# Performance work log

Hardware: AMD Instinct MI355X
Metric: run time of the kernel (lower is better)

The kernel has to match this reference:

```python
import jax, jax.numpy as jnp
import numpy as np

NQ = 6          # num_qubits
BS = 3          # basis_size (Pauli x,y,z)
HID = 32        # LSTM hidden size
SNAPS = 16      # max_num_snapshots
BATCH = 1024
DIM = 2 ** NQ   # 64


def _pauli():
    sx = np.array([[0., 1.], [1., 0.]], dtype=np.complex64)
    sy = np.array([[0., -1j], [1j, 0.]], dtype=np.complex64)
    sz = np.array([[1., 0.], [0., -1.]], dtype=np.complex64)
    return np.stack([sx, sy, sz], axis=0)


def setup_inputs():
    key = jax.random.key(0)
    ks = jax.random.split(key, 12)
    snapshot = jax.random.uniform(ks[0], (BATCH, NQ), jnp.float32, -1.0, 1.0)
    basis_comp_vector = jax.nn.softmax(
        jax.random.normal(ks[1], (BATCH, NQ, BS), jnp.float32), axis=-1)
    # valid density matrices: rho = A A^dag / tr
    ar = jax.random.normal(ks[2], (BATCH, DIM, DIM), jnp.float32)
    ai = jax.random.normal(ks[3], (BATCH, DIM, DIM), jnp.float32)
    A = ar + 1j * ai
    rho_c = jnp.einsum('bij,bkj->bik', A, jnp.conj(A))
    tr = jnp.trace(rho_c, axis1=1, axis2=2)[:, None, None]
    rho_c = rho_c / tr
    rho = jnp.stack([jnp.real(rho_c), jnp.imag(rho_c)], axis=1).astype(jnp.float32)
    h0 = jax.random.normal(ks[4], (BATCH, HID), jnp.float32)
    c0 = jax.random.normal(ks[5], (BATCH, HID), jnp.float32)
    in_dim = NQ + NQ * BS
    W_ih = jax.random.normal(ks[6], (4 * HID, in_dim), jnp.float32) * 0.1
    W_hh = jax.random.normal(ks[7], (4 * HID, HID), jnp.float32) * 0.1
    b_ih = jax.random.normal(ks[8], (4 * HID,), jnp.float32) * 0.05
    b_hh = jax.random.normal(ks[9], (4 * HID,), jnp.float32) * 0.05
    Wp = jax.random.normal(ks[10], (NQ, HID, BS), jnp.float32) * 0.1
    bp = jax.random.normal(ks[11], (NQ, BS), jnp.float32) * 0.05
    pauli = _pauli()
    basis_r = jnp.asarray(np.real(pauli), jnp.float32)
    basis_i = jnp.asarray(np.imag(pauli), jnp.float32)
    return {"snapshot": snapshot, "basis_comp_vector": basis_comp_vector,
            "rho": rho, "h0": h0, "c0": c0,
            "W_ih": W_ih, "W_hh": W_hh, "b_ih": b_ih, "b_hh": b_hh,
            "Wp": Wp, "bp": bp, "basis_r": basis_r, "basis_i": basis_i}


def _apply(p, M, axis, b):
    # apply 2x2 batched operator M [b,2,2] on tensor axis `axis` of p [b]+(2,)*2NQ
    pm = jnp.moveaxis(p, axis, 1)
    shp = pm.shape
    out = jnp.einsum('bij,bjr->bir', M, pm.reshape(b, 2, -1)).reshape(shp)
    return jnp.moveaxis(out, 1, axis)


def _measure(rho_t, probs, basis, basis_c, b):
    # sequential single-qubit measurement on the collapsing mixed state
    pc = probs.astype(jnp.complex64)
    M = jnp.einsum('bqs,sij->bqij', pc, basis)    # prob-mixed basis ops
    Mc = jnp.einsum('bqs,sij->bqij', pc, basis_c)
    p = rho_t
    outs = []
    for q in range(NQ):
        p = _apply(p, M[:, q], 1 + q, b)          # row index of qubit q
        p = _apply(p, Mc[:, q], 1 + NQ + q, b)    # col index of qubit q
        tr = jnp.trace(p.reshape(b, DIM, DIM), axis1=1, axis2=2)
        outs.append(jnp.real(tr))                 # measurement value s
        p = p / tr.reshape((b,) + (1,) * (2 * NQ))  # renormalized post-state
    return jnp.stack(outs, axis=1)                 # [b, NQ]


def _forward(snapshot, basis_comp_vector, rho, h0, c0,
             W_ih, W_hh, b_ih, b_hh, Wp, bp, basis_r, basis_i):
    b = snapshot.shape[0]
    basis = (basis_r + 1j * basis_i).astype(jnp.complex64)
    basis_c = jnp.conj(basis)
    rho_t = (rho[:, 0] + 1j * rho[:, 1]).astype(jnp.complex64)
    rho_t = rho_t.reshape((b,) + (2,) * (2 * NQ))

    x = jnp.concatenate([snapshot, basis_comp_vector.reshape(b, -1)], axis=-1)
    feats = [x]
    h, c = h0, c0
    for _ in range(SNAPS - 1):
        # torch LSTMCell: gate order i, f, g, o
        g = x @ W_ih.T + b_ih + h @ W_hh.T + b_hh
        gi, gf, gg, go = jnp.split(g, 4, axis=-1)
        c = jax.nn.sigmoid(gf) * c + jax.nn.sigmoid(gi) * jnp.tanh(gg)
        h = jax.nn.sigmoid(go) * jnp.tanh(c)
        probs = jax.nn.softmax(jnp.einsum('bh,qhs->bqs', h, Wp) + bp, axis=-1)
        # torch.Tensor(snapshot_batch) detaches -> stop_gradient
        snaps = jax.lax.stop_gradient(_measure(rho_t, probs, basis, basis_c, b))
        x = jnp.concatenate([snaps, probs.reshape(b, -1)], axis=-1)
        feats.append(x)

    # classical-shadow reconstruction: kron_q (I + 3 s_q B_q)/2, averaged
    eye2 = jnp.eye(2, dtype=jnp.complex64)
    acc = jnp.zeros((b, DIM, DIM), jnp.complex64)
    last_bv = None
    for xw in feats:
        shadow = xw[:, :NQ]
        bv = xw[:, NQ:].reshape(b, NQ, BS)
        last_bv = bv
        Bq = jnp.einsum('bqs,sij->bqij', bv.astype(jnp.complex64), basis)
        rc = (eye2 + 3.0 * shadow[:, :, None, None].astype(jnp.complex64) * Bq) / 2.0
        k = rc[:, 0]
        dd = 2
        for q in range(1, NQ):  # batched kron chain
            k = jnp.einsum('bij,bkl->bikjl', k, rc[:, q]).reshape(b, dd * 2, dd * 2)
            dd *= 2
        acc = acc + k
    rho_rec = acc / SNAPS
    out = jnp.stack([jnp.real(rho_rec), jnp.imag(rho_rec)], axis=1)
    return out, last_bv


def reference(snapshot, basis_comp_vector, rho, h0, c0,
              W_ih, W_hh, b_ih, b_hh, Wp, bp, basis_r, basis_i):
    return _forward(snapshot, basis_comp_vector, rho, h0, c0,
                    W_ih, W_hh, b_ih, b_hh, Wp, bp, basis_r, basis_i)
```

## Files before the change

### kernel.cpp

```cpp
#include <hip/hip_runtime.h>

#define NQ 6
#define BS 3
#define HID 32
#define SNAPS 16
#define BATCH 1024
#define XDIM 24
#define G4 128

#define OFF_KA   0
#define OFF_KB   2560
#define OFF_WPT  5120
#define OFF_BP   5768
#define OFF_FEAT 5788
#define OFF_X    6172
#define OFF_H    6196
#define OFF_G    6228
#define SMEM_FLOATS 6356

__device__ __forceinline__ float sigm_f(float x) { return 1.0f / (1.0f + __expf(-x)); }
__device__ __forceinline__ float tanh_f(float x) { return 1.0f - 2.0f / (__expf(2.0f * x) + 1.0f); }

__device__ __forceinline__ void rc_entry(float g, float b0, float b1, float b2,
                                         int i, int j, float& re, float& im) {
    if (i == j) { re = 0.5f + (i ? -g * b2 : g * b2); im = 0.0f; }
    else        { re = g * b0;  im = (i ? g * b1 : -g * b1); }
}

__device__ __forceinline__ void build_K(const float* fx, int half, int a, float* dst) {
    int i0 = (a >> 5) & 1, i1 = (a >> 4) & 1, i2 = (a >> 3) & 1;
    int j0 = (a >> 2) & 1, j1 = (a >> 1) & 1, j2 = a & 1;
    int q = 3 * half;
    float g0 = 1.5f * fx[q], g1 = 1.5f * fx[q + 1], g2 = 1.5f * fx[q + 2];
    const float* bb = fx + 6 + 3 * q;
    float r0, m0, r1, m1, r2, m2;
    rc_entry(g0, bb[0], bb[1], bb[2], i0, j0, r0, m0);
    rc_entry(g1, bb[3], bb[4], bb[5], i1, j1, r1, m1);
    rc_entry(g2, bb[6], bb[7], bb[8], i2, j2, r2, m2);
    float pr = r0 * r1 - m0 * m1, pi = r0 * m1 + m0 * r1;
    float qr = pr * r2 - pi * m2, qi = pr * m2 + pi * r2;
    int idx = (a & 7) * 20 + 2 * (a >> 3);
    dst[idx] = qr; dst[idx + 1] = qi;
}

__global__ __launch_bounds__(256, 4)
void lstm_shadow_kernel(const float* __restrict__ snapshot,
                        const float* __restrict__ bcv,
                        const float* __restrict__ h0,
                        const float* __restrict__ c0,
                        const float* __restrict__ W_ih,
                        const float* __restrict__ W_hh,
                        const float* __restrict__ b_ih,
                        const float* __restrict__ b_hh,
                        const float* __restrict__ Wp,
                        const float* __restrict__ bp,
                        float* __restrict__ out)
{
    __shared__ __align__(16) float smem[SMEM_FLOATS];
    const int b = blockIdx.x;
    const int t = threadIdx.x;

    float* sKA   = smem + OFF_KA;
    float* sKB   = smem + OFF_KB;
    float* sWpT  = smem + OFF_WPT;
    float* sbp   = smem + OFF_BP;
    float* sfeat = smem + OFF_FEAT;
    float* sx    = smem + OFF_X;
    float* sh    = smem + OFF_H;
    float* sg    = smem + OFF_G;

    float4 wih4[6], whh4[8];
    float breg = 0.0f, creg = 0.0f;

    if (t < G4) {
        const float4* wi = (const float4*)(W_ih + t * 24);
        #pragma unroll
        for (int k = 0; k < 6; ++k) wih4[k] = wi[k];
        const float4* wh = (const float4*)(W_hh + t * 32);
        #pragma unroll
        for (int k = 0; k < 8; ++k) whh4[k] = wh[k];
        breg = b_ih[t] + b_hh[t];
    }
    for (int idx = t; idx < NQ * HID * BS; idx += 256) {
        int q = idx / 96, r = idx - q * 96;
        int h = r / 3, s = r - h * 3;
        sWpT[(q * 3 + s) * 36 + h] = Wp[idx];
    }
    if (t < 18) sbp[t] = bp[t];
    if (t < 32) { sh[t] = h0[b * HID + t]; creg = c0[b * HID + t]; }
    if (t < 24) {
        float v = (t < 6) ? snapshot[b * NQ + t] : bcv[b * 18 + (t - 6)];
        sx[t] = v; sfeat[t] = v;
    }
    __syncthreads();

    for (int step = 0; step < SNAPS - 1; ++step) {
        if (t < G4) {
            const float4* sx4 = (const float4*)sx;
            const float4* sh4 = (const float4*)sh;
            float ga = breg, gb = 0.0f;
            #pragma unroll
            for (int k = 0; k < 6; ++k) {
                float4 xq = sx4[k];
                ga += xq.x * wih4[k].x + xq.y * wih4[k].y;
                gb += xq.z * wih4[k].z + xq.w * wih4[k].w;
            }
            #pragma unroll
            for (int k = 0; k < 8; ++k) {
                float4 hq = sh4[k];
                ga += hq.x * whh4[k].x + hq.y * whh4[k].y;
                gb += hq.z * whh4[k].z + hq.w * whh4[k].w;
            }
            sg[t] = ga + gb;
        } else {
            int u = t - G4;
            const float* fx = &sfeat[step * XDIM];
            if (u < 64) build_K(fx, 0, u, &sKA[step * 160]);
            else        build_K(fx, 1, u - 64, &sKB[step * 160]);
        }
        __syncthreads();

        if (t < 64) {
            if (t < 32) {
                float gi = sg[t], gf = sg[32 + t], gg = sg[64 + t], go = sg[96 + t];
                creg = sigm_f(gf) * creg + sigm_f(gi) * tanh_f(gg);
                float hnew = sigm_f(go) * tanh_f(creg);
                sh[t] = hnew;
            }
            __builtin_amdgcn_wave_barrier();
            int row = (t < 18) ? t : 17;
            const float4* wr  = (const float4*)&sWpT[row * 36];
            const float4* sh4 = (const float4*)sh;
            float la = (t < 18) ? sbp[row] : 0.0f, lb = 0.0f;
            #pragma unroll
            for (int c2 = 0; c2 < 8; ++c2) {
                float4 hq = sh4[c2], wq = wr[c2];
                la += hq.x * wq.x + hq.y * wq.y;
                lb += hq.z * wq.z + hq.w * wq.w;
            }
            float l = la + lb;
            int q3 = (t < 6) ? 3 * t : 0;
            float l0 = __shfl(l, q3), l1 = __shfl(l, q3 + 1), l2 = __shfl(l, q3 + 2);
            if (t < 6) {
                float m = fmaxf(l0, fmaxf(l1, l2));
                float e0 = __expf(l0 - m), e1 = __expf(l1 - m), e2 = __expf(l2 - m);
                float inv = 1.0f / (e0 + e1 + e2);
                float p0 = e0 * inv, p1 = e1 * inv, p2 = e2 * inv;
                float snap = p0 * p0 + p1 * p1 + p2 * p2;
                float* fx2 = &sfeat[(step + 1) * XDIM];
                sx[t] = snap;              fx2[t] = snap;
                sx[6 + 3 * t]     = p0;    fx2[6 + 3 * t]     = p0;
                sx[6 + 3 * t + 1] = p1;    fx2[6 + 3 * t + 1] = p1;
                sx[6 + 3 * t + 2] = p2;    fx2[6 + 3 * t + 2] = p2;
            }
        }
        __syncthreads();
    }

    if (t < G4) {
        const float* fx = &sfeat[15 * XDIM];
        if (t < 64) build_K(fx, 0, t, &sKA[15 * 160]);
        else        build_K(fx, 1, t - 64, &sKB[15 * 160]);
    } else if (t < G4 + 18) {
        int u = t - G4;
        out[(size_t)BATCH * 8192 + (size_t)b * 18 + u] = sfeat[15 * XDIM + 6 + u];
    }
    __syncthreads();

    const int w  = t >> 6;
    const int j  = t & 63;
    const int jA = j >> 3;
    const int jB = j & 7;

    float accr[16], acci[16];
    #pragma unroll
    for (int e = 0; e < 16; ++e) { accr[e] = 0.0f; acci[e] = 0.0f; }

    #pragma unroll
    for (int f = 0; f < SNAPS; ++f) {
        const float* KAT = &sKA[f * 160 + jA * 20];
        const float* KBT = &sKB[f * 160 + jB * 20];
        float4 a0 = ((const float4*)KAT)[0];
        float4 a1 = ((const float4*)KAT)[1];
        float4 a2 = ((const float4*)KAT)[2];
        float4 a3 = ((const float4*)KAT)[3];
        float b0r = KBT[2 * w],     b0i = KBT[2 * w + 1];
        float b1r = KBT[2 * w + 8], b1i = KBT[2 * w + 9];
        #define CMAC(m, ar, ai)                              \
            accr[2*(m)]   += (ar)*b0r - (ai)*b0i;            \
            acci[2*(m)]   += (ar)*b0i + (ai)*b0r;            \
            accr[2*(m)+1] += (ar)*b1r - (ai)*b1i;            \
            acci[2*(m)+1] += (ar)*b1i + (ai)*b1r;
        CMAC(0, a0.x, a0.y) CMAC(1, a0.z, a0.w)
        CMAC(2, a1.x, a1.y) CMAC(3, a1.z, a1.w)
        CMAC(4, a2.x, a2.y) CMAC(5, a2.z, a2.w)
        CMAC(6, a3.x, a3.y) CMAC(7, a3.z, a3.w)
        #undef CMAC
    }

    const float inv16 = 1.0f / 16.0f;
    float* outb = out + (size_t)b * 8192;
    #pragma unroll
    for (int e = 0; e < 16; ++e) {
        int idx = e * 256 + t;
        outb[idx]        = accr[e] * inv16;
        outb[4096 + idx] = acci[e] * inv16;
    }
}

extern "C" void kernel_launch(void* const* d_in, const int* in_sizes, int n_in,
                              void* d_out, int out_size, void* d_ws, size_t ws_size,
                              hipStream_t stream) {
    const float* snapshot = (const float*)d_in[0];
    const float* bcv      = (const float*)d_in[1];
    const float* h0       = (const float*)d_in[3];
    const float* c0       = (const float*)d_in[4];
    const float* W_ih     = (const float*)d_in[5];
    const float* W_hh     = (const float*)d_in[6];
    const float* b_ih     = (const float*)d_in[7];
    const float* b_hh     = (const float*)d_in[8];
    const float* Wp       = (const float*)d_in[9];
    const float* bp       = (const float*)d_in[10];
    float* out = (float*)d_out;

    lstm_shadow_kernel<<<BATCH, 256, 0, stream>>>(
        snapshot, bcv, h0, c0, W_ih, W_hh, b_ih, b_hh, Wp, bp, out);
}
```

Baseline: 136.3 us.

## Split LSTM recurrence and shadow reconstruction into separate kernels with wave-per-sample LSTM

```diff
diff --git a/kernel.cpp b/kernel.cpp
--- a/kernel.cpp
+++ b/kernel.cpp
@@ -1,22 +1,13 @@
 #include <hip/hip_runtime.h>
 
 #define NQ 6
-#define BS 3
 #define HID 32
 #define SNAPS 16
 #define BATCH 1024
-#define XDIM 24
-#define G4 128
-
-#define OFF_KA   0
-#define OFF_KB   2560
-#define OFF_WPT  5120
-#define OFF_BP   5768
-#define OFF_FEAT 5788
-#define OFF_X    6172
-#define OFF_H    6196
-#define OFF_G    6228
-#define SMEM_FLOATS 6356
+#define FSTRIDE 24
+#define FTOT 384
+#define KSTR 24
+#define KF   192
 
 __device__ __forceinline__ float sigm_f(float x) { return 1.0f / (1.0f + __expf(-x)); }
 __device__ __forceinline__ float tanh_f(float x) { return 1.0f - 2.0f / (__expf(2.0f * x) + 1.0f); }
@@ -27,184 +18,201 @@
     else        { re = g * b0;  im = (i ? g * b1 : -g * b1); }
 }
 
-__device__ __forceinline__ void build_K(const float* fx, int half, int a, float* dst) {
-    int i0 = (a >> 5) & 1, i1 = (a >> 4) & 1, i2 = (a >> 3) & 1;
-    int j0 = (a >> 2) & 1, j1 = (a >> 1) & 1, j2 = a & 1;
-    int q = 3 * half;
-    float g0 = 1.5f * fx[q], g1 = 1.5f * fx[q + 1], g2 = 1.5f * fx[q + 2];
-    const float* bb = fx + 6 + 3 * q;
-    float r0, m0, r1, m1, r2, m2;
-    rc_entry(g0, bb[0], bb[1], bb[2], i0, j0, r0, m0);
-    rc_entry(g1, bb[3], bb[4], bb[5], i1, j1, r1, m1);
-    rc_entry(g2, bb[6], bb[7], bb[8], i2, j2, r2, m2);
-    float pr = r0 * r1 - m0 * m1, pi = r0 * m1 + m0 * r1;
-    float qr = pr * r2 - pi * m2, qi = pr * m2 + pi * r2;
-    int idx = (a & 7) * 20 + 2 * (a >> 3);
-    dst[idx] = qr; dst[idx + 1] = qi;
+__global__ __launch_bounds__(256)
+void lstm_kernel(const float* __restrict__ snapshot,
+                 const float* __restrict__ bcv,
+                 const float* __restrict__ h0,
+                 const float* __restrict__ c0,
+                 const float* __restrict__ W_ih,
+                 const float* __restrict__ W_hh,
+                 const float* __restrict__ b_ih,
+                 const float* __restrict__ b_hh,
+                 const float* __restrict__ Wp,
+                 const float* __restrict__ bp,
+                 float* __restrict__ feats,
+                 float* __restrict__ out_tail)
+{
+    __shared__ __align__(16) float sxh[4][64];
+    const int w = threadIdx.x >> 6;
+    const int l = threadIdx.x & 63;
+    const int b = blockIdx.x * 4 + w;
+    float* sx = &sxh[w][0];
+    float* sh = &sxh[w][32];
+
+    float4 wih0[6], wih1[6], whh0[8], whh1[8];
+    {
+        const float4* p0 = (const float4*)(W_ih + l * 24);
+        const float4* p1 = (const float4*)(W_ih + (l + 64) * 24);
+        #pragma unroll
+        for (int k = 0; k < 6; ++k) { wih0[k] = p0[k]; wih1[k] = p1[k]; }
+        const float4* q0 = (const float4*)(W_hh + l * 32);
+        const float4* q1 = (const float4*)(W_hh + (l + 64) * 32);
+        #pragma unroll
+        for (int k = 0; k < 8; ++k) { whh0[k] = q0[k]; whh1[k] = q1[k]; }
+    }
+    const float bias0 = b_ih[l] + b_hh[l];
+    const float bias1 = b_ih[l + 64] + b_hh[l + 64];
+
+    float wp[32];
+    float bpv = 0.0f;
+    if (l < 18) {
+        int q = l / 3, s = l - 3 * q;
+        #pragma unroll
+        for (int k = 0; k < 32; ++k) wp[k] = Wp[q * 96 + 3 * k + s];
+        bpv = bp[l];
+    }
+
+    float c = 0.0f;
+    if (l < 32) { c = c0[b * 32 + l]; sh[l] = h0[b * 32 + l]; }
+    if (l < 24) {
+        float v = (l < 6) ? snapshot[b * 6 + l] : bcv[b * 18 + (l - 6)];
+        sx[l] = v;
+        feats[b * FTOT + l] = v;
+    }
+    __builtin_amdgcn_wave_barrier();
+
+    for (int step = 0; step < SNAPS - 1; ++step) {
+        const float4* x4 = (const float4*)sx;
+        const float4* h4 = (const float4*)sh;
+        float g0 = bias0, g1 = bias1, g0b = 0.0f, g1b = 0.0f;
+        #pragma unroll
+        for (int k = 0; k < 6; ++k) {
+            float4 xq = x4[k];
+            g0  += xq.x * wih0[k].x + xq.y * wih0[k].y;
+            g0b += xq.z * wih0[k].z + xq.w * wih0[k].w;
+            g1  += xq.x * wih1[k].x + xq.y * wih1[k].y;
+            g1b += xq.z * wih1[k].z + xq.w * wih1[k].w;
+        }
+        #pragma unroll
+        for (int k = 0; k < 8; ++k) {
+            float4 hq = h4[k];
+            g0  += hq.x * whh0[k].x + hq.y * whh0[k].y;
+            g0b += hq.z * whh0[k].z + hq.w * whh0[k].w;
+            g1  += hq.x * whh1[k].x + hq.y * whh1[k].y;
+            g1b += hq.z * whh1[k].z + hq.w * whh1[k].w;
+        }
+        g0 += g0b; g1 += g1b;
+
+        float gf = __shfl_xor(g0, 32);
+        float go = __shfl_xor(g1, 32);
+        if (l < 32) {
+            c = sigm_f(gf) * c + sigm_f(g0) * tanh_f(g1);
+            sh[l] = sigm_f(go) * tanh_f(c);
+        }
+        __builtin_amdgcn_wave_barrier();
+
+        float logit = bpv;
+        const float4* h4b = (const float4*)sh;
+        #pragma unroll
+        for (int k = 0; k < 8; ++k) {
+            float4 hq = h4b[k];
+            logit += hq.x * wp[4 * k] + hq.y * wp[4 * k + 1]
+                   + hq.z * wp[4 * k + 2] + hq.w * wp[4 * k + 3];
+        }
+
+        int q3 = 3 * (l < 6 ? l : 0);
+        float l0 = __shfl(logit, q3), l1 = __shfl(logit, q3 + 1), l2 = __shfl(logit, q3 + 2);
+        if (l < 6) {
+            float m = fmaxf(l0, fmaxf(l1, l2));
+            float e0 = __expf(l0 - m), e1 = __expf(l1 - m), e2 = __expf(l2 - m);
+            float inv = 1.0f / (e0 + e1 + e2);
+            float p0 = e0 * inv, p1 = e1 * inv, p2 = e2 * inv;
+            float snap = p0 * p0 + p1 * p1 + p2 * p2;
+            sx[l] = snap;
+            sx[6 + 3 * l]     = p0;
+            sx[6 + 3 * l + 1] = p1;
+            sx[6 + 3 * l + 2] = p2;
+            float* fd = feats + b * FTOT + (step + 1) * FSTRIDE;
+            fd[l] = snap;
+            fd[6 + 3 * l]     = p0;
+            fd[6 + 3 * l + 1] = p1;
+            fd[6 + 3 * l + 2] = p2;
+            if (step == SNAPS - 2) {
+                float* ot = out_tail + b * 18 + 3 * l;
+                ot[0] = p0; ot[1] = p1; ot[2] = p2;
+            }
+        }
+        __builtin_amdgcn_wave_barrier();
+    }
 }
 
 __global__ __launch_bounds__(256, 4)
-void lstm_shadow_kernel(const float* __restrict__ snapshot,
-                        const float* __restrict__ bcv,
-                        const float* __restrict__ h0,
-                        const float* __restrict__ c0,
-                        const float* __restrict__ W_ih,
-                        const float* __restrict__ W_hh,
-                        const float* __restrict__ b_ih,
-                        const float* __restrict__ b_hh,
-                        const float* __restrict__ Wp,
-                        const float* __restrict__ bp,
-                        float* __restrict__ out)
+void recon_kernel(const float* __restrict__ feats, float* __restrict__ out)
 {
-    __shared__ __align__(16) float smem[SMEM_FLOATS];
+    __shared__ __align__(16) float sK[2 * 16 * KF + FTOT];
+    float* sKA = sK;
+    float* sKB = sK + 16 * KF;
+    float* sf  = sK + 32 * KF;
     const int b = blockIdx.x;
     const int t = threadIdx.x;
 
-    float* sKA   = smem + OFF_KA;
-    float* sKB   = smem + OFF_KB;
-    float* sWpT  = smem + OFF_WPT;
-    float* sbp   = smem + OFF_BP;
-    float* sfeat = smem + OFF_FEAT;
-    float* sx    = smem + OFF_X;
-    float* sh    = smem + OFF_H;
-    float* sg    = smem + OFF_G;
-
-    float4 wih4[6], whh4[8];
-    float breg = 0.0f, creg = 0.0f;
-
-    if (t < G4) {
-        const float4* wi = (const float4*)(W_ih + t * 24);
-        #pragma unroll
-        for (int k = 0; k < 6; ++k) wih4[k] = wi[k];
-        const float4* wh = (const float4*)(W_hh + t * 32);
-        #pragma unroll
-        for (int k = 0; k < 8; ++k) whh4[k] = wh[k];
-        breg = b_ih[t] + b_hh[t];
-    }
-    for (int idx = t; idx < NQ * HID * BS; idx += 256) {
-        int q = idx / 96, r = idx - q * 96;
-        int h = r / 3, s = r - h * 3;
-        sWpT[(q * 3 + s) * 36 + h] = Wp[idx];
-    }
-    if (t < 18) sbp[t] = bp[t];
-    if (t < 32) { sh[t] = h0[b * HID + t]; creg = c0[b * HID + t]; }
-    if (t < 24) {
-        float v = (t < 6) ? snapshot[b * NQ + t] : bcv[b * 18 + (t - 6)];
-        sx[t] = v; sfeat[t] = v;
-    }
+    sf[t] = feats[b * FTOT + t];
+    if (t < 128) sf[256 + t] = feats[b * FTOT + 256 + t];
     __syncthreads();
 
-    for (int step = 0; step < SNAPS - 1; ++step) {
-        if (t < G4) {
-            const float4* sx4 = (const float4*)sx;
-            const float4* sh4 = (const float4*)sh;
-            float ga = breg, gb = 0.0f;
-            #pragma unroll
-            for (int k = 0; k < 6; ++k) {
-                float4 xq = sx4[k];
-                ga += xq.x * wih4[k].x + xq.y * wih4[k].y;
-                gb += xq.z * wih4[k].z + xq.w * wih4[k].w;
-            }
-            #pragma unroll
-            for (int k = 0; k < 8; ++k) {
-                float4 hq = sh4[k];
-                ga += hq.x * whh4[k].x + hq.y * whh4[k].y;
-                gb += hq.z * whh4[k].z + hq.w * whh4[k].w;
-            }
-            sg[t] = ga + gb;
+    for (int n = t; n < 2048; n += 256) {
+        int f = n >> 7, r = n & 127;
+        int half = r >> 6, a = r & 63;
+        const float* fx = &sf[f * FSTRIDE];
+        int i0 = (a >> 5) & 1, i1 = (a >> 4) & 1, i2 = (a >> 3) & 1;
+        int j0 = (a >> 2) & 1, j1 = (a >> 1) & 1, j2 = a & 1;
+        int q = 3 * half;
+        float g0 = 1.5f * fx[q], g1 = 1.5f * fx[q + 1], g2 = 1.5f * fx[q + 2];
+        const float* bb = fx + 6 + 3 * q;
+        float r0, m0, r1, m1, r2, m2;
+        rc_entry(g0, bb[0], bb[1], bb[2], i0, j0, r0, m0);
+        rc_entry(g1, bb[3], bb[4], bb[5], i1, j1, r1, m1);
+        rc_entry(g2, bb[6], bb[7], bb[8], i2, j2, r2, m2);
+        float pr = r0 * r1 - m0 * m1, pi = r0 * m1 + m0 * r1;
+        float qr = pr * r2 - pi * m2, qi = pr * m2 + pi * r2;
+        int row = a >> 3, col = a & 7;
+        if (half == 0) {
+            int off = f * KF + col * KSTR + ((row & 1) ? (7 + row) : row);
+            sKA[off] = qr; sKA[off + 1] = qi;
         } else {
-            int u = t - G4;
-            const float* fx = &sfeat[step * XDIM];
-            if (u < 64) build_K(fx, 0, u, &sKA[step * 160]);
-            else        build_K(fx, 1, u - 64, &sKB[step * 160]);
-        }
-        __syncthreads();
-
-        if (t < 64) {
-            if (t < 32) {
-                float gi = sg[t], gf = sg[32 + t], gg = sg[64 + t], go = sg[96 + t];
-                creg = sigm_f(gf) * creg + sigm_f(gi) * tanh_f(gg);
-                float hnew = sigm_f(go) * tanh_f(creg);
-                sh[t] = hnew;
-            }
-            __builtin_amdgcn_wave_barrier();
-            int row = (t < 18) ? t : 17;
-            const float4* wr  = (const float4*)&sWpT[row * 36];
-            const float4* sh4 = (const float4*)sh;
-            float la = (t < 18) ? sbp[row] : 0.0f, lb = 0.0f;
-            #pragma unroll
-            for (int c2 = 0; c2 < 8; ++c2) {
-                float4 hq = sh4[c2], wq = wr[c2];
-                la += hq.x * wq.x + hq.y * wq.y;
-                lb += hq.z * wq.z + hq.w * wq.w;
-            }
-            float l = la + lb;
-            int q3 = (t < 6) ? 3 * t : 0;
-            float l0 = __shfl(l, q3), l1 = __shfl(l, q3 + 1), l2 = __shfl(l, q3 + 2);
-            if (t < 6) {
-                float m = fmaxf(l0, fmaxf(l1, l2));
-                float e0 = __expf(l0 - m), e1 = __expf(l1 - m), e2 = __expf(l2 - m);
-                float inv = 1.0f / (e0 + e1 + e2);
-                float p0 = e0 * inv, p1 = e1 * inv, p2 = e2 * inv;
-                float snap = p0 * p0 + p1 * p1 + p2 * p2;
-                float* fx2 = &sfeat[(step + 1) * XDIM];
-                sx[t] = snap;              fx2[t] = snap;
-                sx[6 + 3 * t]     = p0;    fx2[6 + 3 * t]     = p0;
-                sx[6 + 3 * t + 1] = p1;    fx2[6 + 3 * t + 1] = p1;
-                sx[6 + 3 * t + 2] = p2;    fx2[6 + 3 * t + 2] = p2;
-            }
-        }
-        __syncthreads();
-    }
-
-    if (t < G4) {
-        const float* fx = &sfeat[15 * XDIM];
-        if (t < 64) build_K(fx, 0, t, &sKA[15 * 160]);
-        else        build_K(fx, 1, t - 64, &sKB[15 * 160]);
-    } else if (t < G4 + 18) {
-        int u = t - G4;
-        out[(size_t)BATCH * 8192 + (size_t)b * 18 + u] = sfeat[15 * XDIM + 6 + u];
+            int off = f * KF + row * KSTR + 2 * col;
+            sKB[off] = qr; sKB[off + 1] = qi;
+        }
     }
     __syncthreads();
 
-    const int w  = t >> 6;
-    const int j  = t & 63;
-    const int jA = j >> 3;
-    const int jB = j & 7;
-
-    float accr[16], acci[16];
+    const int u = t & 15, v = t >> 4;
+    const float* baseA = sKA + (u >> 1) * KSTR + 8 * (v >> 3);
+    const float* baseB = sKB + (v & 7) * KSTR + 8 * (u & 1);
+    float accr[4][4], acci[4][4];
     #pragma unroll
-    for (int e = 0; e < 16; ++e) { accr[e] = 0.0f; acci[e] = 0.0f; }
+    for (int e = 0; e < 4; ++e)
+        #pragma unroll
+        for (int d = 0; d < 4; ++d) { accr[e][d] = 0.0f; acci[e][d] = 0.0f; }
 
     #pragma unroll
     for (int f = 0; f < SNAPS; ++f) {
-        const float* KAT = &sKA[f * 160 + jA * 20];
-        const float* KBT = &sKB[f * 160 + jB * 20];
-        float4 a0 = ((const float4*)KAT)[0];
-        float4 a1 = ((const float4*)KAT)[1];
-        float4 a2 = ((const float4*)KAT)[2];
-        float4 a3 = ((const float4*)KAT)[3];
-        float b0r = KBT[2 * w],     b0i = KBT[2 * w + 1];
-        float b1r = KBT[2 * w + 8], b1i = KBT[2 * w + 9];
-        #define CMAC(m, ar, ai)                              \
-            accr[2*(m)]   += (ar)*b0r - (ai)*b0i;            \
-            acci[2*(m)]   += (ar)*b0i + (ai)*b0r;            \
-            accr[2*(m)+1] += (ar)*b1r - (ai)*b1i;            \
-            acci[2*(m)+1] += (ar)*b1i + (ai)*b1r;
-        CMAC(0, a0.x, a0.y) CMAC(1, a0.z, a0.w)
-        CMAC(2, a1.x, a1.y) CMAC(3, a1.z, a1.w)
-        CMAC(4, a2.x, a2.y) CMAC(5, a2.z, a2.w)
-        CMAC(6, a3.x, a3.y) CMAC(7, a3.z, a3.w)
-        #undef CMAC
-    }
-
-    const float inv16 = 1.0f / 16.0f;
+        float4 A0 = *(const float4*)(baseA + f * KF);
+        float4 A1 = *(const float4*)(baseA + f * KF + 4);
+        float4 B0 = *(const float4*)(baseB + f * KF);
+        float4 B1 = *(const float4*)(baseB + f * KF + 4);
+        float ar[4] = {A0.x, A0.z, A1.x, A1.z};
+        float ai[4] = {A0.y, A0.w, A1.y, A1.w};
+        float br[4] = {B0.x, B0.z, B1.x, B1.z};
+        float bi[4] = {B0.y, B0.w, B1.y, B1.w};
+        #pragma unroll
+        for (int e = 0; e < 4; ++e)
+            #pragma unroll
+            for (int d = 0; d < 4; ++d) {
+                accr[e][d] += ar[e] * br[d] - ai[e] * bi[d];
+                acci[e][d] += ar[e] * bi[d] + ai[e] * br[d];
+            }
+    }
+
+    const float s = 1.0f / 16.0f;
     float* outb = out + (size_t)b * 8192;
     #pragma unroll
-    for (int e = 0; e < 16; ++e) {
-        int idx = e * 256 + t;
-        outb[idx]        = accr[e] * inv16;
-        outb[4096 + idx] = acci[e] * inv16;
+    for (int e = 0; e < 4; ++e) {
+        int i = v + 16 * e;
+        float4 r4 = make_float4(accr[e][0] * s, accr[e][1] * s, accr[e][2] * s, accr[e][3] * s);
+        float4 i4 = make_float4(acci[e][0] * s, acci[e][1] * s, acci[e][2] * s, acci[e][3] * s);
+        *(float4*)(outb + i * 64 + 4 * u) = r4;
+        *(float4*)(outb + 4096 + i * 64 + 4 * u) = i4;
     }
 }
 
@@ -221,8 +229,11 @@
     const float* b_hh     = (const float*)d_in[8];
     const float* Wp       = (const float*)d_in[9];
     const float* bp       = (const float*)d_in[10];
-    float* out = (float*)d_out;
-
-    lstm_shadow_kernel<<<BATCH, 256, 0, stream>>>(
-        snapshot, bcv, h0, c0, W_ih, W_hh, b_ih, b_hh, Wp, bp, out);
-}
+    float* out   = (float*)d_out;
+    float* featw = (float*)d_ws;
+
+    lstm_kernel<<<BATCH / 4, 256, 0, stream>>>(
+        snapshot, bcv, h0, c0, W_ih, W_hh, b_ih, b_hh, Wp, bp,
+        featw, out + (size_t)BATCH * 8192);
+    recon_kernel<<<BATCH, 256, 0, stream>>>(featw, out);
+}
```

After: 276.0 us. 2.03x slower.
